# Kernel tuning notes

Hardware: AMD Instinct MI355X
Metric: run time of the kernel (lower is better)

Reference implementation:

```python
import jax, jax.numpy as jnp
import numpy as np

B, C, H, W = 4, 256, 64, 64
CI = 128  # inter_channels = in_channels // 2
EPS = 1e-5  # torch BatchNorm default eps


def setup_inputs() -> dict:
    key = jax.random.key(0)
    ks = jax.random.split(key, 8)

    def w(k, shape, s=0.02):
        return jax.random.normal(k, shape, jnp.float32) * s

    return {
        "x": jax.random.normal(ks[0], (B, C, H, W), jnp.float32),
        # theta (Q) linear + BatchNorm1d (inference-mode running stats)
        "theta_w": w(ks[1], (CI, C)), "theta_b": jnp.zeros((CI,), jnp.float32),
        "theta_bn_gamma": jnp.ones((CI,), jnp.float32), "theta_bn_beta": jnp.zeros((CI,), jnp.float32),
        "theta_bn_mean": jnp.zeros((CI,), jnp.float32), "theta_bn_var": jnp.ones((CI,), jnp.float32),
        # phi (K) linear + BatchNorm1d
        "phi_w": w(ks[2], (CI, C)), "phi_b": jnp.zeros((CI,), jnp.float32),
        "phi_bn_gamma": jnp.ones((CI,), jnp.float32), "phi_bn_beta": jnp.zeros((CI,), jnp.float32),
        "phi_bn_mean": jnp.zeros((CI,), jnp.float32), "phi_bn_var": jnp.ones((CI,), jnp.float32),
        # g (V) linear
        "g_w": w(ks[3], (CI, C)), "g_b": jnp.zeros((CI,), jnp.float32),
        # W_z output linear
        "wz_w": w(ks[4], (C, CI)), "wz_b": jnp.zeros((C,), jnp.float32),
        # output BatchNorm2d (gamma nonzero instead of init-0 so output is non-trivial)
        "bn_gamma": w(ks[5], (C,), 0.1), "bn_beta": jnp.zeros((C,), jnp.float32),
        "bn_mean": jnp.zeros((C,), jnp.float32), "bn_var": jnp.ones((C,), jnp.float32),
    }


def _linear(z, w, b):
    # z: [B, N, C], w: [D, C] -> [B, N, D]
    return jnp.einsum('bnc,dc->bnd', z, w) + b


def _bn(z, gamma, beta, mean, var):
    # per-channel affine BN in inference mode, channel on last axis
    return (z - mean) * jax.lax.rsqrt(var + EPS) * gamma + beta


def reference(x, theta_w, theta_b, theta_bn_gamma, theta_bn_beta, theta_bn_mean, theta_bn_var,
              phi_w, phi_b, phi_bn_gamma, phi_bn_beta, phi_bn_mean, phi_bn_var,
              g_w, g_b, wz_w, wz_b, bn_gamma, bn_beta, bn_mean, bn_var):
    b, c, h, w = x.shape
    n = h * w
    ci = theta_w.shape[0]
    scale = float(ci) ** (-0.5)

    x_flat = x.reshape(b, c, n).transpose(0, 2, 1)  # [B, N, C]
    Q = _bn(_linear(x_flat, theta_w, theta_b), theta_bn_gamma, theta_bn_beta, theta_bn_mean, theta_bn_var)
    K = _bn(_linear(x_flat, phi_w, phi_b), phi_bn_gamma, phi_bn_beta, phi_bn_mean, phi_bn_var)
    V = _linear(x_flat, g_w, g_b)  # [B, N, CI]

    # attention computed in fp32 (matches torch amp-disabled block)
    attn = jnp.einsum('bnd,bmd->bnm', Q.astype(jnp.float32), K.astype(jnp.float32)) * scale
    attn = jax.nn.softmax(attn, axis=-1).astype(V.dtype)  # [B, N, N]

    y = jnp.einsum('bnm,bmd->bnd', attn, V)  # [B, N, CI]
    y = jnp.einsum('bnd,cd->bnc', y, wz_w) + wz_b  # [B, N, C]
    y = y.transpose(0, 2, 1).reshape(b, c, h, w)

    # BatchNorm2d (inference mode), channel axis 1
    rstd = jax.lax.rsqrt(bn_var + EPS)
    y = (y - bn_mean[None, :, None, None]) * (rstd * bn_gamma)[None, :, None, None] + bn_beta[None, :, None, None]
    return y + x
```

## Files before the change

### kernel.cpp

```cpp
#include <hip/hip_runtime.h>
#include <stdint.h>

typedef __attribute__((ext_vector_type(8))) short bf16x8;
typedef __attribute__((ext_vector_type(4))) float f32x4;

#define WS_WQKV   0u
#define WS_WZ     196608u
#define WS_SCL    262144u
#define WS_SHF    263680u
#define WS_WZS    265216u
#define WS_WZT    266240u
#define WS_Q      524288u
#define WS_K      (WS_Q  + 4194304u)
#define WS_VT     (WS_K  + 4194304u)
#define WS_Y      (WS_VT + 4194304u)
#define WS_OP     (WS_Y  + 4194304u)
#define WS_LP     (WS_OP + 16777216u)

__device__ __forceinline__ short f2bf(float f) {
  union { float f; uint32_t u; } v; v.f = f;
  uint32_t r = v.u + 0x7fffu + ((v.u >> 16) & 1u);
  return (short)(r >> 16);
}

__device__ __forceinline__ f32x4 mfma16(bf16x8 a, bf16x8 b, f32x4 c) {
  return __builtin_amdgcn_mfma_f32_16x16x32_bf16(a, b, c, 0, 0, 0);
}

__global__ __launch_bounds__(256) void prep_kernel(
    const float* theta_w, const float* phi_w, const float* g_w, const float* wz_w,
    const float* theta_b, const float* tg, const float* tb, const float* tm, const float* tv,
    const float* phi_b,   const float* pg, const float* pb, const float* pm, const float* pv,
    const float* g_b,
    const float* wz_b, const float* bg, const float* bb, const float* bm, const float* bv,
    char* ws) {
  int idx = blockIdx.x * 256 + threadIdx.x;
  short* wqkv = (short*)(ws + WS_WQKV);
  if (idx < 98304) {
    float w;
    if (idx < 32768) w = theta_w[idx];
    else if (idx < 65536) w = phi_w[idx - 32768];
    else w = g_w[idx - 65536];
    wqkv[idx] = f2bf(w);
  }
  if (idx < 32768) ((short*)(ws + WS_WZ))[idx] = f2bf(wz_w[idx]);
  if (idx < 384) {
    float s, t;
    if (idx < 128)      { s = tg[idx] * rsqrtf(tv[idx] + 1e-5f);
                          t = (theta_b[idx] - tm[idx]) * s + tb[idx]; }
    else if (idx < 256) { int d = idx - 128; s = pg[d] * rsqrtf(pv[d] + 1e-5f);
                          t = (phi_b[d] - pm[d]) * s + pb[d]; }
    else                { int d = idx - 256; s = 1.0f; t = g_b[d]; }
    ((float*)(ws + WS_SCL))[idx] = s;
    ((float*)(ws + WS_SHF))[idx] = t;
  }
  if (idx < 256) {
    float s = bg[idx] * rsqrtf(bv[idx] + 1e-5f);
    float t = (wz_b[idx] - bm[idx]) * s + bb[idx];
    ((float*)(ws + WS_WZS))[idx] = s;
    ((float*)(ws + WS_WZT))[idx] = t;
  }
}

__global__ __launch_bounds__(256) void qkv_kernel(const float* __restrict__ x, char* ws) {
  const int dt = blockIdx.x, nt = blockIdx.y, b = blockIdx.z;
  const int t = threadIdx.x;
  __shared__ __attribute__((aligned(16))) short xs[64][264];
  const short* wqkv = (const short*)(ws + WS_WQKV);
  const float* scl = (const float*)(ws + WS_SCL);
  const float* shf = (const float*)(ws + WS_SHF);
  const int n0 = nt * 64;
  #pragma unroll
  for (int i = 0; i < 16; ++i) {
    int chunk = i * 256 + t;
    int c = chunk >> 4, nq = chunk & 15;
    const float4 v = *(const float4*)(x + ((size_t)(b * 256 + c) << 12) + n0 + nq * 4);
    xs[nq * 4 + 0][c] = f2bf(v.x);
    xs[nq * 4 + 1][c] = f2bf(v.y);
    xs[nq * 4 + 2][c] = f2bf(v.z);
    xs[nq * 4 + 3][c] = f2bf(v.w);
  }
  __syncthreads();
  const int wv = t >> 6, l = t & 63, lr = l & 15, q = l >> 4;
  f32x4 acc[4] = {};
  #pragma unroll 2
  for (int kt = 0; kt < 8; ++kt) {
    bf16x8 a = *(const bf16x8*)&xs[wv * 16 + lr][kt * 32 + q * 8];
    #pragma unroll
    for (int s = 0; s < 4; ++s) {
      const short* wp = wqkv + (size_t)(dt * 64 + s * 16 + lr) * 256 + kt * 32 + q * 8;
      bf16x8 bf = *(const bf16x8*)wp;
      acc[s] = mfma16(a, bf, acc[s]);
    }
  }
  #pragma unroll
  for (int s = 0; s < 4; ++s) {
    int dg = dt * 64 + s * 16 + lr;
    float sc = scl[dg], sh = shf[dg];
    short vals[4];
    #pragma unroll
    for (int r = 0; r < 4; ++r) vals[r] = f2bf(acc[s][r] * sc + sh);
    int nbase = n0 + wv * 16 + q * 4;
    if (dg < 128) {
      short* Q = (short*)(ws + WS_Q) + ((size_t)b << 19);
      #pragma unroll
      for (int r = 0; r < 4; ++r) Q[(size_t)(nbase + r) * 128 + dg] = vals[r];
    } else if (dg < 256) {
      short* K = (short*)(ws + WS_K) + ((size_t)b << 19);
      int d = dg - 128;
      #pragma unroll
      for (int r = 0; r < 4; ++r) K[(size_t)(nbase + r) * 128 + d] = vals[r];
    } else {
      short* VT = (short*)(ws + WS_VT) + ((size_t)b << 19);
      int d = dg - 256;
      short4 pk; pk.x = vals[0]; pk.y = vals[1]; pk.z = vals[2]; pk.w = vals[3];
      *(short4*)(VT + ((size_t)d << 12) + nbase) = pk;
    }
  }
}

__global__ __launch_bounds__(256, 3) void attn_kernel(char* ws) {
  const int g = blockIdx.x;
  const int b = (g & 7) >> 1;
  const int idx = ((g >> 3) << 1) | (g & 1);
  const int nt = idx >> 2, mc = idx & 3;
  const int t = threadIdx.x, wv = t >> 6, l = t & 63, lr = l & 15, q = l >> 4;
  __shared__ __attribute__((aligned(16))) short ks[64][136];
  __shared__ __attribute__((aligned(16))) short vs[128][72];
  __shared__ __attribute__((aligned(16))) short ps[4][16][72];
  const short* Q  = (const short*)(ws + WS_Q)  + ((size_t)b << 19);
  const short* K  = (const short*)(ws + WS_K)  + ((size_t)b << 19);
  const short* VT = (const short*)(ws + WS_VT) + ((size_t)b << 19);
  const int n0w = nt * 64 + wv * 16;
  bf16x8 qf[4];
  {
    const short* qp = Q + (size_t)(n0w + lr) * 128 + q * 8;
    #pragma unroll
    for (int kt = 0; kt < 4; ++kt) qf[kt] = *(const bf16x8*)(qp + kt * 32);
  }
  f32x4 o[8] = {};
  float lsum[4] = {0.f, 0.f, 0.f, 0.f};
  const float s2 = 0.08838834764831845f * 1.4426950408889634f;
  const int mbase = mc << 10;

  for (int it = 0; it < 16; ++it) {
    const int m0 = mbase + it * 64;
    __syncthreads();
    #pragma unroll
    for (int i = 0; i < 4; ++i) {
      int chunk = i * 256 + t;
      int row = chunk >> 4, dq = chunk & 15;
      *(uint4*)&ks[row][dq * 8] = *(const uint4*)(K + (size_t)(m0 + row) * 128 + dq * 8);
    }
    #pragma unroll
    for (int i = 0; i < 4; ++i) {
      int chunk = i * 256 + t;
      int row = chunk >> 3, mq = chunk & 7;
      *(uint4*)&vs[row][mq * 8] = *(const uint4*)(VT + ((size_t)row << 12) + m0 + mq * 8);
    }
    __syncthreads();
    f32x4 sacc[4] = {};
    #pragma unroll
    for (int kt = 0; kt < 4; ++kt) {
      #pragma unroll
      for (int s = 0; s < 4; ++s) {
        bf16x8 kf = *(const bf16x8*)&ks[s * 16 + lr][kt * 32 + q * 8];
        sacc[s] = mfma16(qf[kt], kf, sacc[s]);
      }
    }
    float pvv[4][4];
    #pragma unroll
    for (int s = 0; s < 4; ++s)
      #pragma unroll
      for (int r = 0; r < 4; ++r)
        pvv[s][r] = exp2f(sacc[s][r] * s2);
    #pragma unroll
    for (int r = 0; r < 4; ++r)
      lsum[r] += (pvv[0][r] + pvv[1][r]) + (pvv[2][r] + pvv[3][r]);
    #pragma unroll
    for (int s = 0; s < 4; ++s)
      #pragma unroll
      for (int r = 0; r < 4; ++r)
        ps[wv][q * 4 + r][s * 16 + lr] = f2bf(pvv[s][r]);
    bf16x8 pf0 = *(const bf16x8*)&ps[wv][lr][q * 8];
    bf16x8 pf1 = *(const bf16x8*)&ps[wv][lr][32 + q * 8];
    #pragma unroll
    for (int dt = 0; dt < 8; ++dt) {
      bf16x8 vf0 = *(const bf16x8*)&vs[dt * 16 + lr][q * 8];
      o[dt] = mfma16(pf0, vf0, o[dt]);
      bf16x8 vf1 = *(const bf16x8*)&vs[dt * 16 + lr][32 + q * 8];
      o[dt] = mfma16(pf1, vf1, o[dt]);
    }
  }
  const int cb = mc * 4 + b;
  float* LP = (float*)(ws + WS_LP) + ((size_t)cb << 12);
  #pragma unroll
  for (int r = 0; r < 4; ++r) {
    float s = lsum[r];
    s += __shfl_xor(s, 1, 64);
    s += __shfl_xor(s, 2, 64);
    s += __shfl_xor(s, 4, 64);
    s += __shfl_xor(s, 8, 64);
    if (lr == 0) LP[n0w + q * 4 + r] = s;
  }
  short* OPc = (short*)(ws + WS_OP) + ((size_t)cb << 19);
  #pragma unroll
  for (int dt = 0; dt < 8; ++dt)
    #pragma unroll
    for (int r = 0; r < 4; ++r)
      OPc[((size_t)(n0w + q * 4 + r) << 7) + dt * 16 + lr] = f2bf(o[dt][r]);
}

__global__ __launch_bounds__(256) void merge_kernel(char* ws) {
  int gid = blockIdx.x * 256 + threadIdx.x;
  int d8 = (gid & 15) * 8;
  int n  = (gid >> 4) & 4095;
  int b  = gid >> 16;
  const short* OP = (const short*)(ws + WS_OP);
  const float* LP = (const float*)(ws + WS_LP);
  float acc[8] = {};
  float lsum = 0.f;
  #pragma unroll
  for (int mc = 0; mc < 4; ++mc) {
    const short* p = OP + ((size_t)(mc * 4 + b) << 19) + ((size_t)n << 7) + d8;
    uint4 v = *(const uint4*)p;
    uint32_t uu[4] = {v.x, v.y, v.z, v.w};
    #pragma unroll
    for (int w = 0; w < 4; ++w) {
      union { uint32_t u; float f; } lo, hi;
      lo.u = uu[w] << 16; hi.u = uu[w] & 0xffff0000u;
      acc[w * 2 + 0] += lo.f;
      acc[w * 2 + 1] += hi.f;
    }
    lsum += LP[((mc * 4 + b) << 12) + n];
  }
  float inv = 1.0f / lsum;
  short out8[8];
  #pragma unroll
  for (int j = 0; j < 8; ++j) out8[j] = f2bf(acc[j] * inv);
  short* Y = (short*)(ws + WS_Y) + ((size_t)b << 19) + ((size_t)n << 7) + d8;
  *(uint4*)Y = *(uint4*)out8;
}

__global__ __launch_bounds__(256) void proj_kernel(const float* __restrict__ x,
                                                   char* ws, float* __restrict__ out) {
  const int ct = blockIdx.x, nt = blockIdx.y, b = blockIdx.z;
  const int t = threadIdx.x, wv = t >> 6, l = t & 63, lr = l & 15, q = l >> 4;
  __shared__ __attribute__((aligned(16))) short ys[64][136];
  __shared__ __attribute__((aligned(16))) short zs[64][136];
  const short* Y  = (const short*)(ws + WS_Y) + ((size_t)b << 19);
  const short* WZ = (const short*)(ws + WS_WZ);
  const float* wzs = (const float*)(ws + WS_WZS);
  const float* wzt = (const float*)(ws + WS_WZT);
  const int n0 = nt * 64, c0 = ct * 64;
  #pragma unroll
  for (int i = 0; i < 4; ++i) {
    int chunk = i * 256 + t;
    int row = chunk >> 4, dq = chunk & 15;
    *(uint4*)&ys[row][dq * 8] = *(const uint4*)(Y + (size_t)(n0 + row) * 128 + dq * 8);
    *(uint4*)&zs[row][dq * 8] = *(const uint4*)(WZ + (size_t)(c0 + row) * 128 + dq * 8);
  }
  __syncthreads();
  f32x4 acc[4] = {};
  #pragma unroll
  for (int kt = 0; kt < 4; ++kt) {
    bf16x8 a = *(const bf16x8*)&ys[wv * 16 + lr][kt * 32 + q * 8];
    #pragma unroll
    for (int s = 0; s < 4; ++s) {
      bf16x8 bf = *(const bf16x8*)&zs[s * 16 + lr][kt * 32 + q * 8];
      acc[s] = mfma16(a, bf, acc[s]);
    }
  }
  #pragma unroll
  for (int s = 0; s < 4; ++s) {
    int c = c0 + s * 16 + lr;
    float sc = wzs[c], sh = wzt[c];
    int nbase = n0 + wv * 16 + q * 4;
    size_t base = ((size_t)(b * 256 + c) << 12) + nbase;
    float4 xv = *(const float4*)(x + base);
    float4 ov;
    ov.x = acc[s][0] * sc + sh + xv.x;
    ov.y = acc[s][1] * sc + sh + xv.y;
    ov.z = acc[s][2] * sc + sh + xv.z;
    ov.w = acc[s][3] * sc + sh + xv.w;
    *(float4*)(out + base) = ov;
  }
}

extern "C" void kernel_launch(void* const* d_in, const int* in_sizes, int n_in,
                              void* d_out, int out_size, void* d_ws, size_t ws_size,
                              hipStream_t stream) {
  const float* x       = (const float*)d_in[0];
  const float* theta_w = (const float*)d_in[1];
  const float* theta_b = (const float*)d_in[2];
  const float* tg      = (const float*)d_in[3];
  const float* tb      = (const float*)d_in[4];
  const float* tm      = (const float*)d_in[5];
  const float* tv      = (const float*)d_in[6];
  const float* phi_w   = (const float*)d_in[7];
  const float* phi_b   = (const float*)d_in[8];
  const float* pg      = (const float*)d_in[9];
  const float* pb      = (const float*)d_in[10];
  const float* pm      = (const float*)d_in[11];
  const float* pv      = (const float*)d_in[12];
  const float* g_w     = (const float*)d_in[13];
  const float* g_b     = (const float*)d_in[14];
  const float* wz_w    = (const float*)d_in[15];
  const float* wz_b    = (const float*)d_in[16];
  const float* bg      = (const float*)d_in[17];
  const float* bb      = (const float*)d_in[18];
  const float* bm      = (const float*)d_in[19];
  const float* bv      = (const float*)d_in[20];
  char* ws = (char*)d_ws;
  float* out = (float*)d_out;

  prep_kernel<<<384, 256, 0, stream>>>(theta_w, phi_w, g_w, wz_w,
                                       theta_b, tg, tb, tm, tv,
                                       phi_b, pg, pb, pm, pv,
                                       g_b, wz_b, bg, bb, bm, bv, ws);
  qkv_kernel<<<dim3(6, 64, 4), 256, 0, stream>>>(x, ws);
  attn_kernel<<<1024, 256, 0, stream>>>(ws);
  merge_kernel<<<1024, 256, 0, stream>>>(ws);
  proj_kernel<<<dim3(4, 64, 4), 256, 0, stream>>>(x, ws, out);
}
```

Measured before the change: 219.2 us.

## Fuse split-KV merge into projection kernel and retile QKV to avoid redundant x loads

The separate merge kernel is folded into the output projection. Each 16-row block now combines the four partial attention outputs and row sums into shared memory, then projects across all 256 channels while reading Wz directly from global memory. This removes one launch and the Y round trip through memory. The QKV kernel now computes all 384 output features per 32-row tile, so x is read and converted once instead of six times, at the cost of more registers (12 accumulators plus 8 cached A fragments) and fewer, larger blocks.

```diff
diff --git a/kernel.cpp b/kernel.cpp
--- a/kernel.cpp
+++ b/kernel.cpp
@@ -63,44 +63,47 @@
 }
 
 __global__ __launch_bounds__(256) void qkv_kernel(const float* __restrict__ x, char* ws) {
-  const int dt = blockIdx.x, nt = blockIdx.y, b = blockIdx.z;
+  const int nt2 = blockIdx.x, b = blockIdx.y;
   const int t = threadIdx.x;
-  __shared__ __attribute__((aligned(16))) short xs[64][264];
+  __shared__ __attribute__((aligned(16))) short xs[32][264];
   const short* wqkv = (const short*)(ws + WS_WQKV);
   const float* scl = (const float*)(ws + WS_SCL);
   const float* shf = (const float*)(ws + WS_SHF);
-  const int n0 = nt * 64;
-  #pragma unroll
-  for (int i = 0; i < 16; ++i) {
+  const int n0 = nt2 * 32;
+  #pragma unroll
+  for (int i = 0; i < 8; ++i) {
     int chunk = i * 256 + t;
-    int c = chunk >> 4, nq = chunk & 15;
-    const float4 v = *(const float4*)(x + ((size_t)(b * 256 + c) << 12) + n0 + nq * 4);
-    xs[nq * 4 + 0][c] = f2bf(v.x);
-    xs[nq * 4 + 1][c] = f2bf(v.y);
-    xs[nq * 4 + 2][c] = f2bf(v.z);
-    xs[nq * 4 + 3][c] = f2bf(v.w);
+    int c = chunk >> 3, n4 = chunk & 7;
+    const float4 v = *(const float4*)(x + ((size_t)(b * 256 + c) << 12) + n0 + n4 * 4);
+    xs[n4 * 4 + 0][c] = f2bf(v.x);
+    xs[n4 * 4 + 1][c] = f2bf(v.y);
+    xs[n4 * 4 + 2][c] = f2bf(v.z);
+    xs[n4 * 4 + 3][c] = f2bf(v.w);
   }
   __syncthreads();
   const int wv = t >> 6, l = t & 63, lr = l & 15, q = l >> 4;
-  f32x4 acc[4] = {};
-  #pragma unroll 2
+  const int wn = wv & 1, dh = wv >> 1;
+  bf16x8 a[8];
+  #pragma unroll
+  for (int kt = 0; kt < 8; ++kt) a[kt] = *(const bf16x8*)&xs[wn * 16 + lr][kt * 32 + q * 8];
+  f32x4 acc[12] = {};
+  #pragma unroll
   for (int kt = 0; kt < 8; ++kt) {
-    bf16x8 a = *(const bf16x8*)&xs[wv * 16 + lr][kt * 32 + q * 8];
-    #pragma unroll
-    for (int s = 0; s < 4; ++s) {
-      const short* wp = wqkv + (size_t)(dt * 64 + s * 16 + lr) * 256 + kt * 32 + q * 8;
+    #pragma unroll
+    for (int s = 0; s < 12; ++s) {
+      const short* wp = wqkv + (size_t)(dh * 192 + s * 16 + lr) * 256 + kt * 32 + q * 8;
       bf16x8 bf = *(const bf16x8*)wp;
-      acc[s] = mfma16(a, bf, acc[s]);
-    }
-  }
-  #pragma unroll
-  for (int s = 0; s < 4; ++s) {
-    int dg = dt * 64 + s * 16 + lr;
+      acc[s] = mfma16(a[kt], bf, acc[s]);
+    }
+  }
+  #pragma unroll
+  for (int s = 0; s < 12; ++s) {
+    int dg = dh * 192 + s * 16 + lr;
     float sc = scl[dg], sh = shf[dg];
     short vals[4];
     #pragma unroll
     for (int r = 0; r < 4; ++r) vals[r] = f2bf(acc[s][r] * sc + sh);
-    int nbase = n0 + wv * 16 + q * 4;
+    int nbase = n0 + wn * 16 + q * 4;
     if (dg < 128) {
       short* Q = (short*)(ws + WS_Q) + ((size_t)b << 19);
       #pragma unroll
@@ -211,71 +214,62 @@
       OPc[((size_t)(n0w + q * 4 + r) << 7) + dt * 16 + lr] = f2bf(o[dt][r]);
 }
 
-__global__ __launch_bounds__(256) void merge_kernel(char* ws) {
-  int gid = blockIdx.x * 256 + threadIdx.x;
-  int d8 = (gid & 15) * 8;
-  int n  = (gid >> 4) & 4095;
-  int b  = gid >> 16;
+__global__ __launch_bounds__(256) void proj_kernel(const float* __restrict__ x,
+                                                   char* ws, float* __restrict__ out) {
+  const int nt = blockIdx.x, b = blockIdx.y;
+  const int t = threadIdx.x, wv = t >> 6, l = t & 63, lr = l & 15, q = l >> 4;
+  __shared__ __attribute__((aligned(16))) short ys[16][136];
   const short* OP = (const short*)(ws + WS_OP);
   const float* LP = (const float*)(ws + WS_LP);
-  float acc[8] = {};
-  float lsum = 0.f;
-  #pragma unroll
-  for (int mc = 0; mc < 4; ++mc) {
-    const short* p = OP + ((size_t)(mc * 4 + b) << 19) + ((size_t)n << 7) + d8;
-    uint4 v = *(const uint4*)p;
-    uint32_t uu[4] = {v.x, v.y, v.z, v.w};
-    #pragma unroll
-    for (int w = 0; w < 4; ++w) {
-      union { uint32_t u; float f; } lo, hi;
-      lo.u = uu[w] << 16; hi.u = uu[w] & 0xffff0000u;
-      acc[w * 2 + 0] += lo.f;
-      acc[w * 2 + 1] += hi.f;
-    }
-    lsum += LP[((mc * 4 + b) << 12) + n];
-  }
-  float inv = 1.0f / lsum;
-  short out8[8];
-  #pragma unroll
-  for (int j = 0; j < 8; ++j) out8[j] = f2bf(acc[j] * inv);
-  short* Y = (short*)(ws + WS_Y) + ((size_t)b << 19) + ((size_t)n << 7) + d8;
-  *(uint4*)Y = *(uint4*)out8;
-}
-
-__global__ __launch_bounds__(256) void proj_kernel(const float* __restrict__ x,
-                                                   char* ws, float* __restrict__ out) {
-  const int ct = blockIdx.x, nt = blockIdx.y, b = blockIdx.z;
-  const int t = threadIdx.x, wv = t >> 6, l = t & 63, lr = l & 15, q = l >> 4;
-  __shared__ __attribute__((aligned(16))) short ys[64][136];
-  __shared__ __attribute__((aligned(16))) short zs[64][136];
-  const short* Y  = (const short*)(ws + WS_Y) + ((size_t)b << 19);
   const short* WZ = (const short*)(ws + WS_WZ);
   const float* wzs = (const float*)(ws + WS_WZS);
   const float* wzt = (const float*)(ws + WS_WZT);
-  const int n0 = nt * 64, c0 = ct * 64;
-  #pragma unroll
-  for (int i = 0; i < 4; ++i) {
-    int chunk = i * 256 + t;
-    int row = chunk >> 4, dq = chunk & 15;
-    *(uint4*)&ys[row][dq * 8] = *(const uint4*)(Y + (size_t)(n0 + row) * 128 + dq * 8);
-    *(uint4*)&zs[row][dq * 8] = *(const uint4*)(WZ + (size_t)(c0 + row) * 128 + dq * 8);
+  const int n0 = nt * 16;
+  {
+    int row = t >> 4, d8 = (t & 15) * 8;
+    int n = n0 + row;
+    float acc8[8] = {};
+    float lsf = 0.f;
+    #pragma unroll
+    for (int mc = 0; mc < 4; ++mc) {
+      int cb = mc * 4 + b;
+      const short* p = OP + ((size_t)cb << 19) + ((size_t)n << 7) + d8;
+      uint4 v = *(const uint4*)p;
+      uint32_t uu[4] = {v.x, v.y, v.z, v.w};
+      #pragma unroll
+      for (int w = 0; w < 4; ++w) {
+        union { uint32_t u; float f; } lo, hi;
+        lo.u = uu[w] << 16; hi.u = uu[w] & 0xffff0000u;
+        acc8[w * 2 + 0] += lo.f;
+        acc8[w * 2 + 1] += hi.f;
+      }
+      lsf += LP[(cb << 12) + n];
+    }
+    float inv = 1.0f / lsf;
+    short out8[8];
+    #pragma unroll
+    for (int j = 0; j < 8; ++j) out8[j] = f2bf(acc8[j] * inv);
+    *(uint4*)&ys[row][d8] = *(uint4*)out8;
   }
   __syncthreads();
+  bf16x8 a[4];
+  #pragma unroll
+  for (int kt = 0; kt < 4; ++kt) a[kt] = *(const bf16x8*)&ys[lr][kt * 32 + q * 8];
   f32x4 acc[4] = {};
   #pragma unroll
   for (int kt = 0; kt < 4; ++kt) {
-    bf16x8 a = *(const bf16x8*)&ys[wv * 16 + lr][kt * 32 + q * 8];
     #pragma unroll
     for (int s = 0; s < 4; ++s) {
-      bf16x8 bf = *(const bf16x8*)&zs[s * 16 + lr][kt * 32 + q * 8];
-      acc[s] = mfma16(a, bf, acc[s]);
+      const short* wp = WZ + (size_t)(wv * 64 + s * 16 + lr) * 128 + kt * 32 + q * 8;
+      bf16x8 bf = *(const bf16x8*)wp;
+      acc[s] = mfma16(a[kt], bf, acc[s]);
     }
   }
   #pragma unroll
   for (int s = 0; s < 4; ++s) {
-    int c = c0 + s * 16 + lr;
+    int c = wv * 64 + s * 16 + lr;
     float sc = wzs[c], sh = wzt[c];
-    int nbase = n0 + wv * 16 + q * 4;
+    int nbase = n0 + q * 4;
     size_t base = ((size_t)(b * 256 + c) << 12) + nbase;
     float4 xv = *(const float4*)(x + base);
     float4 ov;
@@ -318,8 +312,7 @@
                                        theta_b, tg, tb, tm, tv,
                                        phi_b, pg, pb, pm, pv,
                                        g_b, wz_b, bg, bb, bm, bv, ws);
-  qkv_kernel<<<dim3(6, 64, 4), 256, 0, stream>>>(x, ws);
+  qkv_kernel<<<dim3(128, 4), 256, 0, stream>>>(x, ws);
   attn_kernel<<<1024, 256, 0, stream>>>(ws);
-  merge_kernel<<<1024, 256, 0, stream>>>(ws);
-  proj_kernel<<<dim3(4, 64, 4), 256, 0, stream>>>(x, ws, out);
-}
+  proj_kernel<<<dim3(256, 4), 256, 0, stream>>>(x, ws, out);
+}
```

Result: no change. 216.5 us (-1.2%).
